# Kernel optimization log

Measured on AMD Instinct MI355X. Metric: run time of the kernel, lower is better.

## Reference

```python
import jax, jax.numpy as jnp
import numpy as np

M, N, D, P = 16, 2048, 128, 8192
H = N // D  # 16
MAXLEN = 8448
EPS = 1e-5


def layernorm(x, g, b):
    mu = jnp.mean(x, axis=-1, keepdims=True)
    var = jnp.mean(jnp.square(x - mu), axis=-1, keepdims=True)
    return (x - mu) * jax.lax.rsqrt(var + EPS) * g + b


def setup_inputs() -> dict:
    key = jax.random.key(0)
    ks = jax.random.split(key, 10)
    s = 1.0 / np.sqrt(N)  # keep activations O(1) like trained weights
    return {
        "X": jax.random.normal(ks[0], (M, N), jnp.float32),
        "ln1_g": jnp.ones((N,), jnp.float32),
        "ln1_b": jnp.zeros((N,), jnp.float32),
        "Wq": jax.random.normal(ks[1], (N, N), jnp.float32) * s,
        "Wk": jax.random.normal(ks[2], (N, N), jnp.float32) * s,
        "Wv": jax.random.normal(ks[3], (N, N), jnp.float32) * s,
        "Wo": jax.random.normal(ks[4], (N, N), jnp.float32) * s,
        "ln2_g": jnp.ones((N,), jnp.float32),
        "ln2_b": jnp.zeros((N,), jnp.float32),
        "Wup": jax.random.normal(ks[5], (4 * N, N), jnp.float32) * s,
        "Wdown": jax.random.normal(ks[6], (N, 4 * N), jnp.float32) * (1.0 / np.sqrt(4 * N)),
        "cache_K": jax.random.normal(ks[7], (H, MAXLEN, D), jnp.float32),
        "cache_V": jax.random.normal(ks[8], (H, MAXLEN, D), jnp.float32),
    }


def reference(X, ln1_g, ln1_b, Wq, Wk, Wv, Wo, ln2_g, ln2_b, Wup, Wdown, cache_K, cache_V):
    residual = X
    Xn = layernorm(X, ln1_g, ln1_b)
    # torch Linear: y = x @ W.T
    q = (Xn @ Wq.T).reshape(M, H, D).transpose(1, 0, 2)  # (H,M,D)
    k = (Xn @ Wk.T).reshape(M, H, D).transpose(1, 0, 2)
    v = (Xn @ Wv.T).reshape(M, H, D).transpose(1, 0, 2)
    # KV-cache append
    cache_K = jax.lax.dynamic_update_slice(cache_K, k, (0, P, 0))
    cache_V = jax.lax.dynamic_update_slice(cache_V, v, (0, P, 0))
    Kc = cache_K[:, : P + M, :]  # (H,T,D), T = P+M
    Vc = cache_V[:, : P + M, :]
    scores = jnp.einsum("hmd,htd->hmt", q, Kc) / np.sqrt(D)
    weights = jax.nn.softmax(scores, axis=-1)
    attn = jnp.einsum("hmt,htd->hmd", weights, Vc)  # (H,M,D)
    attn = attn.transpose(1, 0, 2).reshape(M, N)
    X = residual + attn @ Wo.T
    residual = X
    Xn = layernorm(X, ln2_g, ln2_b)
    ffn = jax.nn.gelu(Xn @ Wup.T, approximate=False) @ Wdown.T
    return residual + ffn
```

## Files before the change

kernel.cpp:

```cpp
#include <hip/hip_runtime.h>
#include <hip/hip_bf16.h>
#include <math.h>

#define M_TOK 16
#define NDIM  2048
#define DHEAD 128
#define NHEAD 16
#define MAXLEN 8448
#define FFN   8192
#define TC    128
#define NCH   65
#define LN_EPS 1e-5f
#define RSQRT_D 0.08838834764831845f

#define AS1 __attribute__((address_space(1)))
#define AS3 __attribute__((address_space(3)))

__device__ __forceinline__ void gload_lds16(const float* g, float* l) {
    __builtin_amdgcn_global_load_lds((AS1 void*)g, (AS3 void*)l, 16, 0, 0);
}

template<int H>
__device__ __forceinline__ void fold_step(float* v, int lane, int o) {
    bool hi = (lane & o) != 0;
    #pragma unroll
    for (int i = 0; i < H; ++i) {
        float send = hi ? v[i] : v[i + H];
        float keep = hi ? v[i + H] : v[i];
        v[i] = keep + __shfl_xor(send, o);
    }
}

__device__ __forceinline__ void fold64(float* v, int lane) {
    fold_step<32>(v, lane, 32);
    fold_step<16>(v, lane, 16);
    fold_step<8>(v, lane, 8);
    fold_step<4>(v, lane, 4);
    fold_step<2>(v, lane, 2);
    fold_step<1>(v, lane, 1);
}

template<int KDIM>
__device__ __forceinline__ void gemv_splitk(const float* __restrict__ A,
                                            const float* __restrict__ W,
                                            int col0, int wid, int lane,
                                            float* v) {
    const int kbase = wid * (KDIM / 4);
    const float* wp = W + (size_t)col0 * KDIM + kbase + lane * 4;
    const float* ap = A + kbase + lane * 4;
    #pragma unroll 1
    for (int kc = 0; kc < KDIM / 4; kc += 256) {
        float4 w4[4];
        #pragma unroll
        for (int c = 0; c < 4; ++c)
            w4[c] = *(const float4*)(wp + (size_t)c * KDIM + kc);
        #pragma unroll
        for (int m = 0; m < 16; ++m) {
            float4 x4 = *(const float4*)(ap + (size_t)m * KDIM + kc);
            #pragma unroll
            for (int c = 0; c < 4; ++c) {
                v[m * 4 + c] = fmaf(w4[c].x, x4.x, v[m * 4 + c]);
                v[m * 4 + c] = fmaf(w4[c].y, x4.y, v[m * 4 + c]);
                v[m * 4 + c] = fmaf(w4[c].z, x4.z, v[m * 4 + c]);
                v[m * 4 + c] = fmaf(w4[c].w, x4.w, v[m * 4 + c]);
            }
        }
    }
}

__device__ __forceinline__ float crosswave_reduce(float val, int wid, int lane,
                                                  float (*s_red)[64]) {
    if (wid != 0) s_red[wid - 1][lane] = val;
    __syncthreads();
    return val + s_red[0][lane] + s_red[1][lane] + s_red[2][lane];
}

__global__ __launch_bounds__(256) void k_qkv(const float* __restrict__ Xn,
                                             const float* __restrict__ Wq,
                                             const float* __restrict__ Wk,
                                             const float* __restrict__ Wv,
                                             float* __restrict__ qws,
                                             float* __restrict__ kws,
                                             float* __restrict__ vws) {
    __shared__ float s_red[3][64];
    int tid = threadIdx.x, wid = tid >> 6, lane = tid & 63;
    int b = blockIdx.x;
    int sel = b >> 9;
    int cb = (b & 511) * 4;
    const float* W = (sel == 0) ? Wq : (sel == 1) ? Wk : Wv;
    float* dst = (sel == 0) ? qws : (sel == 1) ? kws : vws;
    float v[64];
    #pragma unroll
    for (int i = 0; i < 64; ++i) v[i] = 0.f;
    gemv_splitk<2048>(Xn, W, cb, wid, lane, v);
    fold64(v, lane);
    float r = crosswave_reduce(v[0], wid, lane, s_red);
    if (wid == 0) {
        int m = lane >> 2, c = lane & 3;
        int gcol = cb + c;
        int h = gcol >> 7, d = gcol & 127;
        dst[(((size_t)h * 16 + m) << 7) + d] = r;
    }
}

__device__ __forceinline__ float gelu_exact(float x) {
    return 0.5f * x * (1.0f + erff(x * 0.7071067811865475f));
}

__global__ __launch_bounds__(256) void k_up(const float* __restrict__ A,
                                            const float* __restrict__ W,
                                            float* __restrict__ out) {
    __shared__ float s_red[3][64];
    int tid = threadIdx.x, wid = tid >> 6, lane = tid & 63;
    int cb = blockIdx.x * 4;
    float v[64];
    #pragma unroll
    for (int i = 0; i < 64; ++i) v[i] = 0.f;
    gemv_splitk<2048>(A, W, cb, wid, lane, v);
    fold64(v, lane);
    float r = crosswave_reduce(v[0], wid, lane, s_red);
    if (wid == 0) {
        int m = lane >> 2, c = lane & 3;
        out[(size_t)m * FFN + cb + c] = gelu_exact(r);
    }
}

template<int KDIM>
__global__ __launch_bounds__(256) void k_resid(const float* __restrict__ A,
                                               const float* __restrict__ W,
                                               const float* __restrict__ R,
                                               float* __restrict__ out) {
    __shared__ float s_red[3][64];
    int tid = threadIdx.x, wid = tid >> 6, lane = tid & 63;
    int cb = blockIdx.x * 4;
    float v[64];
    #pragma unroll
    for (int i = 0; i < 64; ++i) v[i] = 0.f;
    gemv_splitk<KDIM>(A, W, cb, wid, lane, v);
    fold64(v, lane);
    float r = crosswave_reduce(v[0], wid, lane, s_red);
    if (wid == 0) {
        int m = lane >> 2, c = lane & 3;
        int col = cb + c;
        out[(size_t)m * NDIM + col] = R[(size_t)m * NDIM + col] + r;
    }
}

__global__ __launch_bounds__(256) void k_ln(const float* __restrict__ X,
                                            const float* __restrict__ g,
                                            const float* __restrict__ b,
                                            float* __restrict__ out) {
    int row = blockIdx.x, tid = threadIdx.x;
    const float4* xp = (const float4*)(X + (size_t)row * NDIM);
    float4 v0 = xp[tid], v1 = xp[tid + 256];
    float s = v0.x + v0.y + v0.z + v0.w + v1.x + v1.y + v1.z + v1.w;
    float q = v0.x*v0.x + v0.y*v0.y + v0.z*v0.z + v0.w*v0.w
            + v1.x*v1.x + v1.y*v1.y + v1.z*v1.z + v1.w*v1.w;
    #pragma unroll
    for (int o = 32; o; o >>= 1) { s += __shfl_xor(s, o); q += __shfl_xor(q, o); }
    __shared__ float ls[4], lq[4];
    int wid = tid >> 6, lane = tid & 63;
    if (lane == 0) { ls[wid] = s; lq[wid] = q; }
    __syncthreads();
    s = ls[0] + ls[1] + ls[2] + ls[3];
    q = lq[0] + lq[1] + lq[2] + lq[3];
    float mu  = s * (1.f / NDIM);
    float var = q * (1.f / NDIM) - mu * mu;
    float rs  = rsqrtf(var + LN_EPS);
    float4 g0 = ((const float4*)g)[tid], g1 = ((const float4*)g)[tid + 256];
    float4 b0 = ((const float4*)b)[tid], b1 = ((const float4*)b)[tid + 256];
    float4 o0, o1;
    o0.x = (v0.x - mu) * rs * g0.x + b0.x;  o0.y = (v0.y - mu) * rs * g0.y + b0.y;
    o0.z = (v0.z - mu) * rs * g0.z + b0.z;  o0.w = (v0.w - mu) * rs * g0.w + b0.w;
    o1.x = (v1.x - mu) * rs * g1.x + b1.x;  o1.y = (v1.y - mu) * rs * g1.y + b1.y;
    o1.z = (v1.z - mu) * rs * g1.z + b1.z;  o1.w = (v1.w - mu) * rs * g1.w + b1.w;
    float4* op = (float4*)(out + (size_t)row * NDIM);
    op[tid] = o0; op[tid + 256] = o1;
}

__global__ __launch_bounds__(256) void k_attn(const float* __restrict__ cacheK,
                                              const float* __restrict__ cacheV,
                                              const float* __restrict__ qws,
                                              const float* __restrict__ kws,
                                              const float* __restrict__ vws,
                                              float* __restrict__ part,
                                              float* __restrict__ ms) {
    __shared__ float s_k[2][2080];
    __shared__ float s_v[2][2080];
    __shared__ float s_q[16 * 144];
    __shared__ float s_p[16][132];
    int bid = blockIdx.x;
    int h = bid / NCH, c = bid % NCH;
    int nT = (c < NCH - 1) ? TC : M_TOK;
    int NST = nT >> 4;
    const float* Kb = (c < NCH - 1) ? cacheK + ((size_t)h * MAXLEN + (size_t)c * TC) * DHEAD
                                    : kws + (size_t)h * M_TOK * DHEAD;
    const float* Vb = (c < NCH - 1) ? cacheV + ((size_t)h * MAXLEN + (size_t)c * TC) * DHEAD
                                    : vws + (size_t)h * M_TOK * DHEAD;
    int tid = threadIdx.x, w = tid >> 6, lane = tid & 63;
    int tloc = lane & 15, ds = lane >> 4;

    {
        const float4* qp = (const float4*)(qws + (size_t)h * M_TOK * DHEAD);
        #pragma unroll
        for (int i = 0; i < 2; ++i) {
            int g = i * 256 + tid;
            float4 v = qp[g];
            int row = g >> 5, col4 = g & 31;
            *(float4*)&s_q[row * 144 + (col4 >> 3) * 36 + (col4 & 7) * 4] = v;
        }
    }

    auto issue = [&](int slot) {
        if (slot >= 2 * NST) return;
        const float* src; float* dst;
        if (slot < NST) { src = Kb + (size_t)slot * 16 * DHEAD; dst = s_k[slot & 1]; }
        else { int j = slot - NST; src = Vb + (size_t)j * 16 * DHEAD; dst = s_v[j & 1]; }
        #pragma unroll
        for (int k = 0; k < 2; ++k) {
            int j = w * 2 + k;
            gload_lds16(src + j * 256 + lane * 4, dst + j * 260);
        }
    };

    issue(0);
    issue(1);
    const int lastSlot = 2 * NST - 1;

    for (int s = 0; s < NST; ++s) {
        if (s == lastSlot) asm volatile("s_waitcnt vmcnt(0) lgkmcnt(0)" ::: "memory");
        else               asm volatile("s_waitcnt vmcnt(2) lgkmcnt(0)" ::: "memory");
        __builtin_amdgcn_s_barrier();
        const float* kbase = s_k[s & 1] + (tloc >> 1) * 260 + (tloc & 1) * 128 + ds * 32;
        float4 kr[8];
        #pragma unroll
        for (int i = 0; i < 8; ++i) kr[i] = *(const float4*)(kbase + i * 4);
        asm volatile("s_waitcnt lgkmcnt(0)" ::: "memory");
        __builtin_amdgcn_s_barrier();
        issue(s + 2);
        #pragma unroll
        for (int mm = 0; mm < 4; ++mm) {
            int m = w * 4 + mm;
            const float* qrow = s_q + m * 144 + ds * 36;
            float a0 = 0.f, a1 = 0.f, a2 = 0.f, a3 = 0.f;
            #pragma unroll
            for (int i = 0; i < 8; ++i) {
                float4 q4 = *(const float4*)(qrow + i * 4);
                a0 = fmaf(kr[i].x, q4.x, a0); a1 = fmaf(kr[i].y, q4.y, a1);
                a2 = fmaf(kr[i].z, q4.z, a2); a3 = fmaf(kr[i].w, q4.w, a3);
            }
            float s0 = (a0 + a1) + (a2 + a3);
            s0 += __shfl_xor(s0, 16);
            s0 += __shfl_xor(s0, 32);
            if (ds == 0) s_p[m][s * 16 + tloc] = s0 * RSQRT_D;
        }
    }

    asm volatile("s_waitcnt lgkmcnt(0)" ::: "memory");
    __builtin_amdgcn_s_barrier();
    {
        int m2 = tid >> 4, tl = tid & 15;
        float mx = -1e30f;
        for (int t = tl; t < nT; t += 16) mx = fmaxf(mx, s_p[m2][t]);
        #pragma unroll
        for (int o = 8; o; o >>= 1) mx = fmaxf(mx, __shfl_xor(mx, o));
        float sm = 0.f;
        for (int t = tl; t < nT; t += 16) {
            float p = __expf(s_p[m2][t] - mx);
            s_p[m2][t] = p;
            sm += p;
        }
        #pragma unroll
        for (int o = 8; o; o >>= 1) sm += __shfl_xor(sm, o);
        if (tl == 0) {
            float* msp = ms + ((size_t)(h * NCH + c) * 16 + m2) * 2;
            msp[0] = mx; msp[1] = sm;
        }
    }

    float2 acc[4] = {{0.f,0.f},{0.f,0.f},{0.f,0.f},{0.f,0.f}};
    for (int j = 0; j < NST; ++j) {
        int s = NST + j;
        if (s == lastSlot) asm volatile("s_waitcnt vmcnt(0) lgkmcnt(0)" ::: "memory");
        else               asm volatile("s_waitcnt vmcnt(2) lgkmcnt(0)" ::: "memory");
        __builtin_amdgcn_s_barrier();
        float2 vr[16];
        const float* vbase = s_v[j & 1];
        #pragma unroll
        for (int r = 0; r < 16; ++r)
            vr[r] = *(const float2*)(vbase + (r >> 1) * 260 + (r & 1) * 128 + lane * 2);
        asm volatile("s_waitcnt lgkmcnt(0)" ::: "memory");
        __builtin_amdgcn_s_barrier();
        issue(s + 2);
        #pragma unroll
        for (int mm = 0; mm < 4; ++mm) {
            int m = w * 4 + mm;
            const float* prow = &s_p[m][j * 16];
            #pragma unroll
            for (int g4 = 0; g4 < 4; ++g4) {
                float4 p4 = *(const float4*)(prow + g4 * 4);
                acc[mm].x = fmaf(p4.x, vr[g4*4+0].x, acc[mm].x);
                acc[mm].y = fmaf(p4.x, vr[g4*4+0].y, acc[mm].y);
                acc[mm].x = fmaf(p4.y, vr[g4*4+1].x, acc[mm].x);
                acc[mm].y = fmaf(p4.y, vr[g4*4+1].y, acc[mm].y);
                acc[mm].x = fmaf(p4.z, vr[g4*4+2].x, acc[mm].x);
                acc[mm].y = fmaf(p4.z, vr[g4*4+2].y, acc[mm].y);
                acc[mm].x = fmaf(p4.w, vr[g4*4+3].x, acc[mm].x);
                acc[mm].y = fmaf(p4.w, vr[g4*4+3].y, acc[mm].y);
            }
        }
    }

    float* dp = part + (((size_t)(h * NCH + c) * 16) + w * 4) * DHEAD + 2 * lane;
    #pragma unroll
    for (int mm = 0; mm < 4; ++mm)
        *(float2*)(dp + (size_t)mm * DHEAD) = acc[mm];
}

__global__ __launch_bounds__(256) void k_combine(const float* __restrict__ part,
                                                 const float* __restrict__ ms,
                                                 float* __restrict__ attnout) {
    __shared__ float s_scale[16][NCH + 3];
    int h = blockIdx.x >> 3, dblk = blockIdx.x & 7;
    int tid = threadIdx.x;
    {
        int cl = tid & 15, m = tid >> 4;
        float gmax = -1e30f;
        for (int c = cl; c < NCH; c += 16)
            gmax = fmaxf(gmax, ms[((size_t)(h * NCH + c) * 16 + m) * 2]);
        #pragma unroll
        for (int o = 8; o; o >>= 1) gmax = fmaxf(gmax, __shfl_xor(gmax, o));
        float denom = 0.f;
        for (int c = cl; c < NCH; c += 16) {
            const float* msp = ms + ((size_t)(h * NCH + c) * 16 + m) * 2;
            denom += msp[1] * __expf(msp[0] - gmax);
        }
        #pragma unroll
        for (int o = 8; o; o >>= 1) denom += __shfl_xor(denom, o);
        float inv = 1.f / denom;
        for (int c = cl; c < NCH; c += 16) {
            const float* msp = ms + ((size_t)(h * NCH + c) * 16 + m) * 2;
            s_scale[m][c] = __expf(msp[0] - gmax) * inv;
        }
    }
    __syncthreads();
    int m = tid >> 4, dd = tid & 15;
    int d = dblk * 16 + dd;
    const float* pp = part + ((size_t)h * NCH * 16 + m) * DHEAD + d;
    float acc = 0.f;
    #pragma unroll 4
    for (int c = 0; c < NCH; ++c)
        acc = fmaf(pp[(size_t)c * 16 * DHEAD], s_scale[m][c], acc);
    attnout[(size_t)m * NDIM + h * DHEAD + d] = acc;
}

extern "C" void kernel_launch(void* const* d_in, const int* in_sizes, int n_in,
                              void* d_out, int out_size, void* d_ws, size_t ws_size,
                              hipStream_t stream) {
    const float* X      = (const float*)d_in[0];
    const float* ln1_g  = (const float*)d_in[1];
    const float* ln1_b  = (const float*)d_in[2];
    const float* Wq     = (const float*)d_in[3];
    const float* Wk     = (const float*)d_in[4];
    const float* Wv     = (const float*)d_in[5];
    const float* Wo     = (const float*)d_in[6];
    const float* ln2_g  = (const float*)d_in[7];
    const float* ln2_b  = (const float*)d_in[8];
    const float* Wup    = (const float*)d_in[9];
    const float* Wdown  = (const float*)d_in[10];
    const float* cacheK = (const float*)d_in[11];
    const float* cacheV = (const float*)d_in[12];
    float* out = (float*)d_out;

    float* ws = (float*)d_ws;
    float* Xn1    = ws;
    float* qws    = Xn1 + 32768;
    float* kws    = qws + 32768;
    float* vws    = kws + 32768;
    float* partb  = vws + 32768;
    float* msb    = partb + 2129920;
    float* attn_o = msb + 33280;
    float* X2     = attn_o + 32768;
    float* Xn2    = X2 + 32768;
    float* ffnh   = Xn2 + 32768;

    k_ln<<<M_TOK, 256, 0, stream>>>(X, ln1_g, ln1_b, Xn1);
    k_qkv<<<1536, 256, 0, stream>>>(Xn1, Wq, Wk, Wv, qws, kws, vws);
    k_attn<<<NHEAD * NCH, 256, 0, stream>>>(cacheK, cacheV, qws, kws, vws, partb, msb);
    k_combine<<<NHEAD * 8, 256, 0, stream>>>(partb, msb, attn_o);
    k_resid<2048><<<512, 256, 0, stream>>>(attn_o, Wo, X, X2);
    k_ln<<<M_TOK, 256, 0, stream>>>(X2, ln2_g, ln2_b, Xn2);
    k_up<<<2048, 256, 0, stream>>>(Xn2, Wup, ffnh);
    k_resid<8192><<<512, 256, 0, stream>>>(ffnh, Wdown, X2, out);
}
```

Measured before the change: 155.6 us.

## Stage GEMV weights and activations through LDS with double-buffered async loads

```diff
diff --git a/kernel.cpp b/kernel.cpp
--- a/kernel.cpp
+++ b/kernel.cpp
@@ -31,48 +31,62 @@
     }
 }
 
-__device__ __forceinline__ void fold64(float* v, int lane) {
-    fold_step<32>(v, lane, 32);
-    fold_step<16>(v, lane, 16);
-    fold_step<8>(v, lane, 8);
-    fold_step<4>(v, lane, 4);
-    fold_step<2>(v, lane, 2);
-    fold_step<1>(v, lane, 1);
+__device__ __forceinline__ void fold16(float* v, int lane) {
+    fold_step<8>(v, lane, 32);
+    fold_step<4>(v, lane, 16);
+    fold_step<2>(v, lane, 8);
+    fold_step<1>(v, lane, 4);
+    v[0] += __shfl_xor(v[0], 2);
+    v[0] += __shfl_xor(v[0], 1);
 }
 
 template<int KDIM>
-__device__ __forceinline__ void gemv_splitk(const float* __restrict__ A,
+__device__ __forceinline__ void gemv_core16(const float* __restrict__ A,
                                             const float* __restrict__ W,
-                                            int col0, int wid, int lane,
-                                            float* v) {
-    const int kbase = wid * (KDIM / 4);
-    const float* wp = W + (size_t)col0 * KDIM + kbase + lane * 4;
-    const float* ap = A + kbase + lane * 4;
+                                            int cb, int w, int lane,
+                                            float* sbuf, float* acc) {
+    constexpr int NS = KDIM / 256;
+    const float* wsrc = W + (size_t)(cb + w) * KDIM + lane * 4;
+    auto issue = [&](int s) {
+        if (s >= NS) return;
+        float* dst = sbuf + (s & 1) * 5120;
+        gload_lds16(wsrc + s * 256, dst + w * 256);
+        #pragma unroll
+        for (int j = 0; j < 4; ++j) {
+            int m = w * 4 + j;
+            gload_lds16(A + (size_t)m * KDIM + s * 256 + lane * 4,
+                        dst + 1024 + m * 256);
+        }
+    };
+    issue(0);
+    issue(1);
     #pragma unroll 1
-    for (int kc = 0; kc < KDIM / 4; kc += 256) {
-        float4 w4[4];
+    for (int s = 0; s < NS; ++s) {
+        if (s == NS - 1) asm volatile("s_waitcnt vmcnt(0) lgkmcnt(0)" ::: "memory");
+        else             asm volatile("s_waitcnt vmcnt(5) lgkmcnt(0)" ::: "memory");
+        __builtin_amdgcn_s_barrier();
+        const float* buf = sbuf + (s & 1) * 5120;
+        float4 wr[4], xr[4];
         #pragma unroll
         for (int c = 0; c < 4; ++c)
-            w4[c] = *(const float4*)(wp + (size_t)c * KDIM + kc);
-        #pragma unroll
-        for (int m = 0; m < 16; ++m) {
-            float4 x4 = *(const float4*)(ap + (size_t)m * KDIM + kc);
+            wr[c] = *(const float4*)(buf + c * 256 + lane * 4);
+        #pragma unroll
+        for (int j = 0; j < 4; ++j)
+            xr[j] = *(const float4*)(buf + 1024 + (w * 4 + j) * 256 + lane * 4);
+        asm volatile("s_waitcnt lgkmcnt(0)" ::: "memory");
+        __builtin_amdgcn_s_barrier();
+        issue(s + 2);
+        #pragma unroll
+        for (int j = 0; j < 4; ++j) {
             #pragma unroll
             for (int c = 0; c < 4; ++c) {
-                v[m * 4 + c] = fmaf(w4[c].x, x4.x, v[m * 4 + c]);
-                v[m * 4 + c] = fmaf(w4[c].y, x4.y, v[m * 4 + c]);
-                v[m * 4 + c] = fmaf(w4[c].z, x4.z, v[m * 4 + c]);
-                v[m * 4 + c] = fmaf(w4[c].w, x4.w, v[m * 4 + c]);
+                acc[j*4+c] = fmaf(wr[c].x, xr[j].x, acc[j*4+c]);
+                acc[j*4+c] = fmaf(wr[c].y, xr[j].y, acc[j*4+c]);
+                acc[j*4+c] = fmaf(wr[c].z, xr[j].z, acc[j*4+c]);
+                acc[j*4+c] = fmaf(wr[c].w, xr[j].w, acc[j*4+c]);
             }
         }
     }
-}
-
-__device__ __forceinline__ float crosswave_reduce(float val, int wid, int lane,
-                                                  float (*s_red)[64]) {
-    if (wid != 0) s_red[wid - 1][lane] = val;
-    __syncthreads();
-    return val + s_red[0][lane] + s_red[1][lane] + s_red[2][lane];
 }
 
 __global__ __launch_bounds__(256) void k_qkv(const float* __restrict__ Xn,
@@ -82,24 +96,25 @@
                                              float* __restrict__ qws,
                                              float* __restrict__ kws,
                                              float* __restrict__ vws) {
-    __shared__ float s_red[3][64];
-    int tid = threadIdx.x, wid = tid >> 6, lane = tid & 63;
+    __shared__ float sbuf[2 * 5120];
+    int tid = threadIdx.x, w = tid >> 6, lane = tid & 63;
     int b = blockIdx.x;
     int sel = b >> 9;
     int cb = (b & 511) * 4;
     const float* W = (sel == 0) ? Wq : (sel == 1) ? Wk : Wv;
     float* dst = (sel == 0) ? qws : (sel == 1) ? kws : vws;
-    float v[64];
-    #pragma unroll
-    for (int i = 0; i < 64; ++i) v[i] = 0.f;
-    gemv_splitk<2048>(Xn, W, cb, wid, lane, v);
-    fold64(v, lane);
-    float r = crosswave_reduce(v[0], wid, lane, s_red);
-    if (wid == 0) {
-        int m = lane >> 2, c = lane & 3;
+    float acc[16];
+    #pragma unroll
+    for (int i = 0; i < 16; ++i) acc[i] = 0.f;
+    gemv_core16<2048>(Xn, W, cb, w, lane, sbuf, acc);
+    fold16(acc, lane);
+    if ((lane & 3) == 0) {
+        int idx = lane >> 2;
+        int j = idx >> 2, c = idx & 3;
+        int m = w * 4 + j;
         int gcol = cb + c;
-        int h = gcol >> 7, d = gcol & 127;
-        dst[(((size_t)h * 16 + m) << 7) + d] = r;
+        int hh = gcol >> 7, d = gcol & 127;
+        dst[(((size_t)hh * 16 + m) << 7) + d] = acc[0];
     }
 }
 
@@ -110,18 +125,19 @@
 __global__ __launch_bounds__(256) void k_up(const float* __restrict__ A,
                                             const float* __restrict__ W,
                                             float* __restrict__ out) {
-    __shared__ float s_red[3][64];
-    int tid = threadIdx.x, wid = tid >> 6, lane = tid & 63;
+    __shared__ float sbuf[2 * 5120];
+    int tid = threadIdx.x, w = tid >> 6, lane = tid & 63;
     int cb = blockIdx.x * 4;
-    float v[64];
-    #pragma unroll
-    for (int i = 0; i < 64; ++i) v[i] = 0.f;
-    gemv_splitk<2048>(A, W, cb, wid, lane, v);
-    fold64(v, lane);
-    float r = crosswave_reduce(v[0], wid, lane, s_red);
-    if (wid == 0) {
-        int m = lane >> 2, c = lane & 3;
-        out[(size_t)m * FFN + cb + c] = gelu_exact(r);
+    float acc[16];
+    #pragma unroll
+    for (int i = 0; i < 16; ++i) acc[i] = 0.f;
+    gemv_core16<2048>(A, W, cb, w, lane, sbuf, acc);
+    fold16(acc, lane);
+    if ((lane & 3) == 0) {
+        int idx = lane >> 2;
+        int j = idx >> 2, c = idx & 3;
+        int m = w * 4 + j;
+        out[(size_t)m * FFN + cb + c] = gelu_exact(acc[0]);
     }
 }
 
@@ -130,19 +146,20 @@
                                                const float* __restrict__ W,
                                                const float* __restrict__ R,
                                                float* __restrict__ out) {
-    __shared__ float s_red[3][64];
-    int tid = threadIdx.x, wid = tid >> 6, lane = tid & 63;
+    __shared__ float sbuf[2 * 5120];
+    int tid = threadIdx.x, w = tid >> 6, lane = tid & 63;
     int cb = blockIdx.x * 4;
-    float v[64];
-    #pragma unroll
-    for (int i = 0; i < 64; ++i) v[i] = 0.f;
-    gemv_splitk<KDIM>(A, W, cb, wid, lane, v);
-    fold64(v, lane);
-    float r = crosswave_reduce(v[0], wid, lane, s_red);
-    if (wid == 0) {
-        int m = lane >> 2, c = lane & 3;
+    float acc[16];
+    #pragma unroll
+    for (int i = 0; i < 16; ++i) acc[i] = 0.f;
+    gemv_core16<KDIM>(A, W, cb, w, lane, sbuf, acc);
+    fold16(acc, lane);
+    if ((lane & 3) == 0) {
+        int idx = lane >> 2;
+        int j = idx >> 2, c = idx & 3;
+        int m = w * 4 + j;
         int col = cb + c;
-        out[(size_t)m * NDIM + col] = R[(size_t)m * NDIM + col] + r;
+        out[(size_t)m * NDIM + col] = R[(size_t)m * NDIM + col] + acc[0];
     }
 }
 
@@ -178,16 +195,15 @@
     op[tid] = o0; op[tid + 256] = o1;
 }
 
-__global__ __launch_bounds__(256) void k_attn(const float* __restrict__ cacheK,
-                                              const float* __restrict__ cacheV,
-                                              const float* __restrict__ qws,
-                                              const float* __restrict__ kws,
-                                              const float* __restrict__ vws,
-                                              float* __restrict__ part,
-                                              float* __restrict__ ms) {
+__global__ __launch_bounds__(256, 2) void k_attn(const float* __restrict__ cacheK,
+                                                 const float* __restrict__ cacheV,
+                                                 const float* __restrict__ qws,
+                                                 const float* __restrict__ kws,
+                                                 const float* __restrict__ vws,
+                                                 float* __restrict__ part,
+                                                 float* __restrict__ ms) {
     __shared__ float s_k[2][2080];
     __shared__ float s_v[2][2080];
-    __shared__ float s_q[16 * 144];
     __shared__ float s_p[16][132];
     int bid = blockIdx.x;
     int h = bid / NCH, c = bid % NCH;
@@ -200,16 +216,17 @@
     int tid = threadIdx.x, w = tid >> 6, lane = tid & 63;
     int tloc = lane & 15, ds = lane >> 4;
 
+    float4 qreg[4][8];
     {
         const float4* qp = (const float4*)(qws + (size_t)h * M_TOK * DHEAD);
         #pragma unroll
-        for (int i = 0; i < 2; ++i) {
-            int g = i * 256 + tid;
-            float4 v = qp[g];
-            int row = g >> 5, col4 = g & 31;
-            *(float4*)&s_q[row * 144 + (col4 >> 3) * 36 + (col4 & 7) * 4] = v;
-        }
-    }
+        for (int mm = 0; mm < 4; ++mm) {
+            #pragma unroll
+            for (int i = 0; i < 8; ++i)
+                qreg[mm][i] = qp[(size_t)(w * 4 + mm) * 32 + ds * 8 + i];
+        }
+    }
+    asm volatile("s_waitcnt vmcnt(0)" ::: "memory");
 
     auto issue = [&](int slot) {
         if (slot >= 2 * NST) return;
@@ -240,19 +257,18 @@
         issue(s + 2);
         #pragma unroll
         for (int mm = 0; mm < 4; ++mm) {
-            int m = w * 4 + mm;
-            const float* qrow = s_q + m * 144 + ds * 36;
             float a0 = 0.f, a1 = 0.f, a2 = 0.f, a3 = 0.f;
             #pragma unroll
             for (int i = 0; i < 8; ++i) {
-                float4 q4 = *(const float4*)(qrow + i * 4);
-                a0 = fmaf(kr[i].x, q4.x, a0); a1 = fmaf(kr[i].y, q4.y, a1);
-                a2 = fmaf(kr[i].z, q4.z, a2); a3 = fmaf(kr[i].w, q4.w, a3);
+                a0 = fmaf(kr[i].x, qreg[mm][i].x, a0);
+                a1 = fmaf(kr[i].y, qreg[mm][i].y, a1);
+                a2 = fmaf(kr[i].z, qreg[mm][i].z, a2);
+                a3 = fmaf(kr[i].w, qreg[mm][i].w, a3);
             }
             float s0 = (a0 + a1) + (a2 + a3);
             s0 += __shfl_xor(s0, 16);
             s0 += __shfl_xor(s0, 32);
-            if (ds == 0) s_p[m][s * 16 + tloc] = s0 * RSQRT_D;
+            if (ds == 0) s_p[w * 4 + mm][s * 16 + tloc] = s0 * RSQRT_D;
         }
     }
 
```

Result: faster. 144.6 us (-7.1%).
